# Kernel tuning notes

Hardware: AMD Instinct MI355X
Metric: run time of the kernel (lower is better)

## Reference

```python
import jax, jax.numpy as jnp
import numpy as np

NEG_SLOPE = 0.2
BN_EPS = 1e-5
NUM_GRAPHS = 500


def gat_conv(x, src, dst, W, att_src, att_dst, bias, num_nodes):
    # x: [N, Fin], W: [Fin, H*C], att_*: [H, C], bias: [H*C]
    H, C = att_src.shape
    xh = (x @ W).reshape(num_nodes, H, C)                      # [N,H,C]
    a_src = jnp.einsum('nhc,hc->nh', xh, att_src)              # [N,H]
    a_dst = jnp.einsum('nhc,hc->nh', xh, att_dst)              # [N,H]
    e = jax.nn.leaky_relu(a_src[src] + a_dst[dst], NEG_SLOPE)  # [E,H]
    m = jax.ops.segment_max(e, dst, num_segments=num_nodes)    # [N,H]
    m = jnp.where(jnp.isfinite(m), m, 0.0)
    ee = jnp.exp(e - m[dst])
    s = jax.ops.segment_sum(ee, dst, num_segments=num_nodes)   # [N,H]
    alpha = ee / (s[dst] + 1e-16)                              # [E,H]
    out = jax.ops.segment_sum(alpha[:, :, None] * xh[src], dst,
                              num_segments=num_nodes)          # [N,H,C]
    return out.reshape(num_nodes, H * C) + bias


def bn_eval(x, gamma, beta, rmean, rvar):
    return (x - rmean) * jax.lax.rsqrt(rvar + BN_EPS) * gamma + beta


def setup_inputs() -> dict:
    key = jax.random.key(0)
    ks = jax.random.split(key, 24)
    N, E, F_in, A = 50000, 1600000, 32, 16
    inp = {
        'x': jax.random.normal(ks[0], (N, F_in), jnp.float32),
        'edge_index': jax.random.randint(ks[1], (2, E), 0, N, jnp.int32),
        'batch': jnp.sort(jax.random.randint(ks[2], (N,), 0, NUM_GRAPHS, jnp.int32)),
        'W1': jax.random.normal(ks[3], (F_in, 64), jnp.float32) * 0.1,
        'att_src1': jax.random.normal(ks[4], (4, 16), jnp.float32) * 0.1,
        'att_dst1': jax.random.normal(ks[5], (4, 16), jnp.float32) * 0.1,
        'b1': jnp.zeros((64,), jnp.float32),
        'bn1_g': jnp.ones((64,), jnp.float32),
        'bn1_b': jnp.zeros((64,), jnp.float32),
        'bn1_rm': jax.random.normal(ks[6], (64,), jnp.float32) * 0.1,
        'bn1_rv': jax.random.uniform(ks[7], (64,), jnp.float32) + 0.5,
        'W2': jax.random.normal(ks[8], (64, 128), jnp.float32) * 0.1,
        'att_src2': jax.random.normal(ks[9], (4, 32), jnp.float32) * 0.1,
        'att_dst2': jax.random.normal(ks[10], (4, 32), jnp.float32) * 0.1,
        'b2': jnp.zeros((128,), jnp.float32),
        'bn2_g': jnp.ones((128,), jnp.float32),
        'bn2_b': jnp.zeros((128,), jnp.float32),
        'bn2_rm': jax.random.normal(ks[11], (128,), jnp.float32) * 0.1,
        'bn2_rv': jax.random.uniform(ks[12], (128,), jnp.float32) + 0.5,
        # attention pooling gate
        'gate_W': jax.random.normal(ks[13], (128, 1), jnp.float32) * 0.1,
        'gate_b': jnp.zeros((1,), jnp.float32),
        # heads
        'fc1_W': jax.random.normal(ks[14], (128, 32), jnp.float32) * 0.1,
        'fc1_b': jnp.zeros((32,), jnp.float32),
        'val_W': jax.random.normal(ks[15], (32, 1), jnp.float32) * 0.1,
        'val_b': jnp.zeros((1,), jnp.float32),
        'adv_W': jax.random.normal(ks[16], (32, A), jnp.float32) * 0.1,
        'adv_b': jnp.zeros((A,), jnp.float32),
    }
    return inp


def reference(x, edge_index, batch, W1, att_src1, att_dst1, b1,
              bn1_g, bn1_b, bn1_rm, bn1_rv,
              W2, att_src2, att_dst2, b2,
              bn2_g, bn2_b, bn2_rm, bn2_rv,
              gate_W, gate_b, fc1_W, fc1_b,
              val_W, val_b, adv_W, adv_b):
    N = x.shape[0]
    # GATConv default add_self_loops=True
    loop = jnp.arange(N, dtype=edge_index.dtype)
    src = jnp.concatenate([edge_index[0], loop])
    dst = jnp.concatenate([edge_index[1], loop])

    h = gat_conv(x, src, dst, W1, att_src1, att_dst1, b1, N)
    h = jax.nn.relu(bn_eval(h, bn1_g, bn1_b, bn1_rm, bn1_rv))
    h = gat_conv(h, src, dst, W2, att_src2, att_dst2, b2, N)
    h = jax.nn.relu(bn_eval(h, bn2_g, bn2_b, bn2_rm, bn2_rv))

    # AttentionalAggregation: softmax(gate) over nodes per graph, weighted sum
    gate = h @ gate_W + gate_b                                  # [N,1]
    gmax = jax.ops.segment_max(gate, batch, num_segments=NUM_GRAPHS)
    gmax = jnp.where(jnp.isfinite(gmax), gmax, 0.0)
    ge = jnp.exp(gate - gmax[batch])
    gs = jax.ops.segment_sum(ge, batch, num_segments=NUM_GRAPHS)
    w = ge / (gs[batch] + 1e-16)                                # [N,1]
    pooled = jax.ops.segment_sum(w * h, batch, num_segments=NUM_GRAPHS)  # [G,128]

    z = jax.nn.relu(pooled @ fc1_W + fc1_b)
    value = z @ val_W + val_b                                   # [G,1]
    adv = z @ adv_W + adv_b                                     # [G,A]
    return value + (adv - adv.mean(axis=1, keepdims=True))
```

## Files before the change

### kernel.cpp

```cpp
#include <hip/hip_runtime.h>
#include <hip/hip_fp16.h>
#include <math.h>

#define NEG_SLOPE 0.2f
#define BN_EPS_F 1e-5f
#define NUM_G 500
#define NBUK_MAX 128
#define CHUNK 4096

typedef float v2f __attribute__((ext_vector_type(2)));

__device__ __forceinline__ float leaky(float x){ return x > 0.f ? x : NEG_SLOPE*x; }
__device__ __forceinline__ float bcast(float v, int k){
  return __int_as_float(__builtin_amdgcn_readlane(__float_as_int(v), k));
}

#define HB 256
#define BB 64
#define L1B 512
__global__ __launch_bounds__(256) void fused_hist_lin1_kernel(
    const int* __restrict__ edst, int E, int* __restrict__ bukcnt,
    int bshift, int nbuk,
    const int* __restrict__ batch, int* __restrict__ gcnt,
    const float* __restrict__ x, const float* __restrict__ W,
    const float* __restrict__ att_s, const float* __restrict__ att_d,
    unsigned char* __restrict__ xh, float* __restrict__ a_src, float* __restrict__ a_dst, int N)
{
  __shared__ int lhist[NUM_G];
  int t = threadIdx.x;
  int bid = blockIdx.x;
  if (bid < HB) {
    if (t < NBUK_MAX) lhist[t] = 0;
    __syncthreads();
    int i = bid*256 + t, stride = HB*256;
    for (; i < E; i += stride) atomicAdd(&lhist[edst[i] >> bshift], 1);
    __syncthreads();
    if (t < nbuk && lhist[t]) atomicAdd(&bukcnt[t], lhist[t]);
  } else if (bid < HB + BB) {
    for (int i = t; i < NUM_G; i += 256) lhist[i] = 0;
    __syncthreads();
    int i = (bid-HB)*256 + t, stride = BB*256;
    for (; i < N; i += stride) atomicAdd(&lhist[batch[i]], 1);
    __syncthreads();
    for (int i = t; i < NUM_G; i += 256) if (lhist[i]) atomicAdd(&gcnt[i], lhist[i]);
  } else {
    int lane = t & 63;
    int wid  = ((bid - HB - BB)*256 + t) >> 6;
    int nw   = (L1B*256) >> 6;
    float w[32];
    #pragma unroll
    for (int k = 0; k < 32; ++k) w[k] = W[k*64 + lane];
    float asv = att_s[lane], adv = att_d[lane];
    for (int n = wid; n < N; n += nw) {
      float xv = (lane < 32) ? x[(size_t)n*32 + lane] : 0.f;
      float acc = 0.f;
      #pragma unroll
      for (int k = 0; k < 32; ++k) acc = fmaf(bcast(xv, k), w[k], acc);
      float sv = acc*asv, dv = acc*adv;
      #pragma unroll
      for (int m = 1; m < 16; m <<= 1) { sv += __shfl_xor(sv, m); dv += __shfl_xor(dv, m); }
      float accp = __shfl_xor(acc, 1);
      if ((lane & 1) == 0) {
        int p = __builtin_amdgcn_cvt_pk_fp8_f32(acc, accp, 0, false);
        *(unsigned short*)(xh + (size_t)n*64 + lane) = (unsigned short)(p & 0xffff);
      }
      if ((lane & 15) == 0) { a_src[n*4 + (lane>>4)] = sv; a_dst[n*4 + (lane>>4)] = dv; }
    }
  }
}

__global__ __launch_bounds__(1024) void exscan2_kernel(
    const int* __restrict__ in0, int* __restrict__ out0, int n0,
    const int* __restrict__ in1, int* __restrict__ out1, int n1)
{
  const int* in  = blockIdx.x ? in1  : in0;
  int*       out = blockIdx.x ? out1 : out0;
  int        n   = blockIdx.x ? n1   : n0;
  __shared__ int part[1024];
  int t = threadIdx.x;
  int per = (n + 1023) >> 10;
  int lo = t*per, hi = lo + per; if (lo > n) lo = n; if (hi > n) hi = n;
  int s = 0;
  for (int i = lo; i < hi; ++i) s += in[i];
  part[t] = s;
  __syncthreads();
  for (int ofs = 1; ofs < 1024; ofs <<= 1) {
    int v = (t >= ofs) ? part[t-ofs] : 0;
    __syncthreads();
    part[t] += v;
    __syncthreads();
  }
  int base = part[t] - s;
  for (int i = lo; i < hi; ++i) { out[i] = base; base += in[i]; }
  if (t == 1023) out[n] = part[1023];
}

__global__ __launch_bounds__(256) void binscat_kernel(
    const int* __restrict__ esrc, const int* __restrict__ edst, int E,
    const int* __restrict__ bukoff, int* __restrict__ bukcur,
    int2* __restrict__ pairs, int bshift, int nbuk)
{
  __shared__ int hist[NBUK_MAX];
  __shared__ int loffs[NBUK_MAX];
  __shared__ int gbase[NBUK_MAX];
  __shared__ int2 stage[CHUNK];
  int t = threadIdx.x;
  for (int c0 = blockIdx.x*CHUNK; c0 < E; c0 += gridDim.x*CHUNK) {
    int cnt = E - c0; if (cnt > CHUNK) cnt = CHUNK;
    if (t < NBUK_MAX) hist[t] = 0;
    __syncthreads();
    for (int i = t; i < cnt; i += 256)
      atomicAdd(&hist[edst[c0+i] >> bshift], 1);
    __syncthreads();
    int cb = (t < nbuk) ? hist[t] : 0;
    for (int ofs = 1; ofs < nbuk; ofs <<= 1) {
      int v = (t < nbuk && t >= ofs) ? hist[t-ofs] : 0;
      __syncthreads();
      if (t < nbuk) hist[t] += v;
      __syncthreads();
    }
    if (t < nbuk) {
      int lo = hist[t] - cb;
      loffs[t] = lo;
      int base = atomicAdd(&bukcur[t], cb);
      gbase[t] = bukoff[t] + base - lo;
    }
    __syncthreads();
    if (t < nbuk) hist[t] = 0;
    __syncthreads();
    for (int i = t; i < cnt; i += 256) {
      int s = esrc[c0+i], d = edst[c0+i];
      int b = d >> bshift;
      int r = atomicAdd(&hist[b], 1);
      stage[loffs[b] + r] = make_int2(s, d);
    }
    __syncthreads();
    for (int j = t; j < cnt; j += 256) {
      int2 p = stage[j];
      pairs[gbase[p.y >> bshift] + j] = p;
    }
    __syncthreads();
  }
}

__global__ __launch_bounds__(512) void bucket_csr_kernel(
    const int2* __restrict__ pairs, const int* __restrict__ bukoff,
    int* __restrict__ off, int* __restrict__ csr, int N, int E, int bshift)
{
  __shared__ int cnt[1024];
  __shared__ int cur[1024];
  __shared__ int part[512];
  int b = blockIdx.x, t = threadIdx.x;
  int base = b << bshift;
  int bnodes = 1 << bshift;
  int nlocal = N - base; if (nlocal > bnodes) nlocal = bnodes;
  int lo = bukoff[b], hi = bukoff[b+1];
  int gb = lo;
  for (int i = t; i < bnodes; i += 512) cnt[i] = 0;
  __syncthreads();
  for (int i = lo + t; i < hi; i += 512) atomicAdd(&cnt[pairs[i].y - base], 1);
  __syncthreads();
  int Wc = bnodes >> 9;
  int mys = 0;
  for (int j = 0; j < Wc; ++j) mys += cnt[t*Wc + j];
  part[t] = mys;
  __syncthreads();
  for (int ofs = 1; ofs < 512; ofs <<= 1) {
    int v = (t >= ofs) ? part[t-ofs] : 0;
    __syncthreads();
    part[t] += v;
    __syncthreads();
  }
  int ex = part[t] - mys;
  for (int j = 0; j < Wc; ++j) { int c = cnt[t*Wc + j]; cnt[t*Wc + j] = ex; ex += c; }
  __syncthreads();
  for (int i = t; i < nlocal; i += 512) off[base + i] = gb + cnt[i];
  if (b == 0 && t == 0) off[N] = E;
  for (int i = t; i < bnodes; i += 512) cur[i] = 0;
  __syncthreads();
  for (int i = lo + t; i < hi; i += 512) {
    int2 p = pairs[i];
    int l = p.y - base;
    int pos = gb + cnt[l] + atomicAdd(&cur[l], 1);
    csr[pos] = p.x;
  }
}

__global__ __launch_bounds__(256) void gat_agg1_kernel(
    const unsigned char* __restrict__ xh, const float* __restrict__ a_src, const float* __restrict__ a_dst,
    const int* __restrict__ off, const int* __restrict__ csr,
    const float* __restrict__ bias, const float* __restrict__ bng, const float* __restrict__ bnb,
    const float* __restrict__ bnrm, const float* __restrict__ bnrv,
    float* __restrict__ hout, int N)
{
  int lane = threadIdx.x & 63;
  int wid  = (blockIdx.x * blockDim.x + threadIdx.x) >> 6;
  int nw   = (gridDim.x * blockDim.x) >> 6;
  int g  = lane >> 4;
  int li = lane & 15;
  int c0 = li * 4;
  int h  = li >> 2;
  float sc[4], of[4];
  #pragma unroll
  for (int j = 0; j < 4; ++j) {
    sc[j] = rsqrtf(bnrv[c0+j]+BN_EPS_F) * bng[c0+j];
    of[j] = bias[c0+j]*sc[j] + bnb[c0+j] - bnrm[c0+j]*sc[j];
  }
  for (int n = wid; n < N; n += nw) {
    int lo = off[n], hi = off[n+1];
    float adh = a_dst[n*4+h];
    float es  = __expf(leaky(a_src[n*4+h] + adh));
    float acc0=0.f, acc1=0.f, acc2=0.f, acc3=0.f, ssum=0.f;
    for (int e = lo; e < hi; e += 4) {
      int ee = e + g; bool ok = ee < hi;
      int s = __builtin_nontemporal_load(csr + (ok ? ee : lo));
      float a = a_src[s*4+h];
      unsigned int rw = *(const unsigned int*)(xh + (size_t)s*64 + c0);
      float w = ok ? __expf(leaky(a+adh)) : 0.f;
      ssum += w;
      v2f flo = __builtin_amdgcn_cvt_pk_f32_fp8(rw, false);
      v2f fhi = __builtin_amdgcn_cvt_pk_f32_fp8(rw, true);
      acc0 = fmaf(w, flo.x, acc0); acc1 = fmaf(w, flo.y, acc1);
      acc2 = fmaf(w, fhi.x, acc2); acc3 = fmaf(w, fhi.y, acc3);
    }
    #pragma unroll
    for (int m = 16; m < 64; m <<= 1) {
      acc0 += __shfl_xor(acc0, m); acc1 += __shfl_xor(acc1, m);
      acc2 += __shfl_xor(acc2, m); acc3 += __shfl_xor(acc3, m);
      ssum += __shfl_xor(ssum, m);
    }
    unsigned int rw = *(const unsigned int*)(xh + (size_t)n*64 + c0);
    v2f flo = __builtin_amdgcn_cvt_pk_f32_fp8(rw, false);
    v2f fhi = __builtin_amdgcn_cvt_pk_f32_fp8(rw, true);
    acc0 = fmaf(es, flo.x, acc0); acc1 = fmaf(es, flo.y, acc1);
    acc2 = fmaf(es, fhi.x, acc2); acc3 = fmaf(es, fhi.y, acc3);
    ssum += es;
    float inv = 1.f / (ssum + 1e-16f);
    if (g == 0) {
      float4 r;
      r.x = fmaxf(fmaf(acc0*inv, sc[0], of[0]), 0.f);
      r.y = fmaxf(fmaf(acc1*inv, sc[1], of[1]), 0.f);
      r.z = fmaxf(fmaf(acc2*inv, sc[2], of[2]), 0.f);
      r.w = fmaxf(fmaf(acc3*inv, sc[3], of[3]), 0.f);
      *(float4*)(hout + (size_t)n*64 + c0) = r;
    }
  }
}

__global__ __launch_bounds__(256) void lin2_kernel(
    const float* __restrict__ hin, const float* __restrict__ W,
    const float* __restrict__ att_s, const float* __restrict__ att_d,
    unsigned char* __restrict__ xh, float* __restrict__ a_src, float* __restrict__ a_dst, int N)
{
  int lane = threadIdx.x & 63;
  int wid  = (blockIdx.x * blockDim.x + threadIdx.x) >> 6;
  int nw   = (gridDim.x * blockDim.x) >> 6;
  float wa[64], wb[64];
  #pragma unroll
  for (int k = 0; k < 64; ++k) { wa[k] = W[k*128 + lane]; wb[k] = W[k*128 + 64 + lane]; }
  float asa = att_s[lane], ada = att_d[lane];
  float asb = att_s[64+lane], adb = att_d[64+lane];
  for (int n = wid; n < N; n += nw) {
    float hv = hin[(size_t)n*64 + lane];
    float a0 = 0.f, a1 = 0.f;
    #pragma unroll
    for (int k = 0; k < 64; ++k) {
      float h = bcast(hv, k);
      a0 = fmaf(h, wa[k], a0); a1 = fmaf(h, wb[k], a1);
    }
    float sva = a0*asa, dva = a0*ada, svb = a1*asb, dvb = a1*adb;
    #pragma unroll
    for (int m = 1; m < 32; m <<= 1) {
      sva += __shfl_xor(sva, m); dva += __shfl_xor(dva, m);
      svb += __shfl_xor(svb, m); dvb += __shfl_xor(dvb, m);
    }
    float b0 = __shfl_xor(a0, 1);
    float b1 = __shfl_xor(a1, 1);
    if ((lane & 1) == 0) {
      int p0 = __builtin_amdgcn_cvt_pk_fp8_f32(a0, b0, 0, false);
      int p1 = __builtin_amdgcn_cvt_pk_fp8_f32(a1, b1, 0, false);
      *(unsigned short*)(xh + (size_t)n*128 + lane)      = (unsigned short)(p0 & 0xffff);
      *(unsigned short*)(xh + (size_t)n*128 + 64 + lane) = (unsigned short)(p1 & 0xffff);
    }
    if ((lane & 31) == 0) {
      int hh = lane >> 5;
      a_src[n*4 + hh] = sva;     a_dst[n*4 + hh] = dva;
      a_src[n*4 + 2 + hh] = svb; a_dst[n*4 + 2 + hh] = dvb;
    }
  }
}

__global__ __launch_bounds__(256) void gat_agg2_kernel(
    const unsigned char* __restrict__ xh, const float* __restrict__ a_src, const float* __restrict__ a_dst,
    const int* __restrict__ off, const int* __restrict__ csr,
    const float* __restrict__ bias, const float* __restrict__ bng, const float* __restrict__ bnb,
    const float* __restrict__ bnrm, const float* __restrict__ bnrv,
    const float* __restrict__ gateW, const float* __restrict__ gateB,
    float* __restrict__ hout, float* __restrict__ gate, int N)
{
  int lane = threadIdx.x & 63;
  int wid  = (blockIdx.x * blockDim.x + threadIdx.x) >> 6;
  int nw   = (gridDim.x * blockDim.x) >> 6;
  int g  = lane >> 4;
  int li = lane & 15;
  int c0 = li * 8;
  int h  = li >> 2;
  float sc[8], of[8], gw[8];
  #pragma unroll
  for (int j = 0; j < 8; ++j) {
    sc[j] = rsqrtf(bnrv[c0+j]+BN_EPS_F) * bng[c0+j];
    of[j] = bias[c0+j]*sc[j] + bnb[c0+j] - bnrm[c0+j]*sc[j];
    gw[j] = gateW[c0+j];
  }
  float gb = gateB[0];
  for (int n = wid; n < N; n += nw) {
    int lo = off[n], hi = off[n+1];
    float adh = a_dst[n*4+h];
    float es  = __expf(leaky(a_src[n*4+h] + adh));
    float acc0=0.f, acc1=0.f, acc2=0.f, acc3=0.f;
    float acc4=0.f, acc5=0.f, acc6=0.f, acc7=0.f, ssum=0.f;
    for (int e = lo; e < hi; e += 4) {
      int ee = e + g; bool ok = ee < hi;
      int s = __builtin_nontemporal_load(csr + (ok ? ee : lo));
      float a = a_src[s*4+h];
      int2 rv = *(const int2*)(xh + (size_t)s*128 + c0);
      float w = ok ? __expf(leaky(a+adh)) : 0.f;
      ssum += w;
      v2f f0 = __builtin_amdgcn_cvt_pk_f32_fp8((unsigned)rv.x, false);
      v2f f1 = __builtin_amdgcn_cvt_pk_f32_fp8((unsigned)rv.x, true);
      v2f f2 = __builtin_amdgcn_cvt_pk_f32_fp8((unsigned)rv.y, false);
      v2f f3 = __builtin_amdgcn_cvt_pk_f32_fp8((unsigned)rv.y, true);
      acc0 = fmaf(w, f0.x, acc0); acc1 = fmaf(w, f0.y, acc1);
      acc2 = fmaf(w, f1.x, acc2); acc3 = fmaf(w, f1.y, acc3);
      acc4 = fmaf(w, f2.x, acc4); acc5 = fmaf(w, f2.y, acc5);
      acc6 = fmaf(w, f3.x, acc6); acc7 = fmaf(w, f3.y, acc7);
    }
    #pragma unroll
    for (int m = 16; m < 64; m <<= 1) {
      acc0 += __shfl_xor(acc0, m); acc1 += __shfl_xor(acc1, m);
      acc2 += __shfl_xor(acc2, m); acc3 += __shfl_xor(acc3, m);
      acc4 += __shfl_xor(acc4, m); acc5 += __shfl_xor(acc5, m);
      acc6 += __shfl_xor(acc6, m); acc7 += __shfl_xor(acc7, m);
      ssum += __shfl_xor(ssum, m);
    }
    int2 rv = *(const int2*)(xh + (size_t)n*128 + c0);
    v2f f0 = __builtin_amdgcn_cvt_pk_f32_fp8((unsigned)rv.x, false);
    v2f f1 = __builtin_amdgcn_cvt_pk_f32_fp8((unsigned)rv.x, true);
    v2f f2 = __builtin_amdgcn_cvt_pk_f32_fp8((unsigned)rv.y, false);
    v2f f3 = __builtin_amdgcn_cvt_pk_f32_fp8((unsigned)rv.y, true);
    acc0 = fmaf(es, f0.x, acc0); acc1 = fmaf(es, f0.y, acc1);
    acc2 = fmaf(es, f1.x, acc2); acc3 = fmaf(es, f1.y, acc3);
    acc4 = fmaf(es, f2.x, acc4); acc5 = fmaf(es, f2.y, acc5);
    acc6 = fmaf(es, f3.x, acc6); acc7 = fmaf(es, f3.y, acc7);
    ssum += es;
    float inv = 1.f / (ssum + 1e-16f);
    float r0 = fmaxf(fmaf(acc0*inv, sc[0], of[0]), 0.f);
    float r1 = fmaxf(fmaf(acc1*inv, sc[1], of[1]), 0.f);
    float r2 = fmaxf(fmaf(acc2*inv, sc[2], of[2]), 0.f);
    float r3 = fmaxf(fmaf(acc3*inv, sc[3], of[3]), 0.f);
    float r4 = fmaxf(fmaf(acc4*inv, sc[4], of[4]), 0.f);
    float r5 = fmaxf(fmaf(acc5*inv, sc[5], of[5]), 0.f);
    float r6 = fmaxf(fmaf(acc6*inv, sc[6], of[6]), 0.f);
    float r7 = fmaxf(fmaf(acc7*inv, sc[7], of[7]), 0.f);
    if (g == 0) {
      float4 w0 = make_float4(r0, r1, r2, r3);
      float4 w1 = make_float4(r4, r5, r6, r7);
      *(float4*)(hout + (size_t)n*128 + c0)     = w0;
      *(float4*)(hout + (size_t)n*128 + c0 + 4) = w1;
    }
    float gl = r0*gw[0] + r1*gw[1] + r2*gw[2] + r3*gw[3]
             + r4*gw[4] + r5*gw[5] + r6*gw[6] + r7*gw[7];
    #pragma unroll
    for (int m = 1; m < 16; m <<= 1) gl += __shfl_xor(gl, m);
    if (lane == 0) gate[n] = gl + gb;
  }
}

__global__ __launch_bounds__(128) void pool_kernel(
    const float* __restrict__ h2, const float* __restrict__ gate, const int* __restrict__ goff,
    const float* __restrict__ fc1W, const float* __restrict__ fc1b,
    const float* __restrict__ valW, const float* __restrict__ valb,
    const float* __restrict__ advW, const float* __restrict__ advb,
    float* __restrict__ out)
{
  int g = blockIdx.x, t = threadIdx.x;
  int lo = goff[g], hi = goff[g+1];
  __shared__ float red[2];
  __shared__ float pld[128];
  __shared__ float zs[32];
  __shared__ float sval;
  __shared__ float adv_s[16];

  float m = -3.4e38f;
  for (int n = lo+t; n < hi; n += 128) m = fmaxf(m, gate[n]);
  #pragma unroll
  for (int msk = 1; msk < 64; msk <<= 1) m = fmaxf(m, __shfl_xor(m, msk));
  if ((t & 63) == 0) red[t >> 6] = m;
  __syncthreads();
  m = fmaxf(red[0], red[1]);
  __syncthreads();
  float sl = 0.f;
  for (int n = lo+t; n < hi; n += 128) sl += __expf(gate[n]-m);
  #pragma unroll
  for (int msk = 1; msk < 64; msk <<= 1) sl += __shfl_xor(sl, msk);
  if ((t & 63) == 0) red[t >> 6] = sl;
  __syncthreads();
  float s = red[0] + red[1];
  float acc = 0.f;
  for (int n = lo; n < hi; ++n) {
    float w = __expf(gate[n]-m);
    acc += w * h2[(size_t)n*128 + t];
  }
  pld[t] = acc / (s + 1e-16f);
  __syncthreads();
  if (t < 32) {
    float z = fc1b[t];
    #pragma unroll 4
    for (int k = 0; k < 128; ++k) z += pld[k]*fc1W[k*32 + t];
    zs[t] = fmaxf(z, 0.f);
  }
  __syncthreads();
  if (t < 32) {
    float pv = zs[t]*valW[t];
    #pragma unroll
    for (int msk = 1; msk < 32; msk <<= 1) pv += __shfl_xor(pv, msk);
    if (t == 0) sval = pv + valb[0];
  }
  if (t < 16) {
    float a = advb[t];
    #pragma unroll
    for (int k = 0; k < 32; ++k) a += zs[k]*advW[k*16 + t];
    adv_s[t] = a;
  }
  __syncthreads();
  if (t < 16) {
    float amean = adv_s[t];
    #pragma unroll
    for (int msk = 1; msk < 16; msk <<= 1) amean += __shfl_xor(amean, msk);
    amean *= (1.f/16.f);
    out[g*16 + t] = sval + adv_s[t] - amean;
  }
}

extern "C" void kernel_launch(void* const* d_in, const int* in_sizes, int n_in,
                              void* d_out, int out_size, void* d_ws, size_t ws_size,
                              hipStream_t stream)
{
  const float* x     = (const float*)d_in[0];
  const int*   eidx  = (const int*)  d_in[1];
  const int*   batch = (const int*)  d_in[2];
  const float* W1    = (const float*)d_in[3];
  const float* as1w  = (const float*)d_in[4];
  const float* ad1w  = (const float*)d_in[5];
  const float* b1    = (const float*)d_in[6];
  const float* bn1g  = (const float*)d_in[7];
  const float* bn1b  = (const float*)d_in[8];
  const float* bn1rm = (const float*)d_in[9];
  const float* bn1rv = (const float*)d_in[10];
  const float* W2    = (const float*)d_in[11];
  const float* as2w  = (const float*)d_in[12];
  const float* ad2w  = (const float*)d_in[13];
  const float* b2    = (const float*)d_in[14];
  const float* bn2g  = (const float*)d_in[15];
  const float* bn2b  = (const float*)d_in[16];
  const float* bn2rm = (const float*)d_in[17];
  const float* bn2rv = (const float*)d_in[18];
  const float* gateW = (const float*)d_in[19];
  const float* gateB = (const float*)d_in[20];
  const float* fc1W  = (const float*)d_in[21];
  const float* fc1b  = (const float*)d_in[22];
  const float* valW  = (const float*)d_in[23];
  const float* valb  = (const float*)d_in[24];
  const float* advW  = (const float*)d_in[25];
  const float* advb  = (const float*)d_in[26];

  int N = in_sizes[0] / 32;
  int E = in_sizes[1] / 2;
  const int* esrc = eidx;
  const int* edst = eidx + E;

  int bshift = 9;
  while ((((N - 1) >> bshift) + 1) > NBUK_MAX) ++bshift;
  int nbuk = ((N - 1) >> bshift) + 1;

  float* ws = (float*)d_ws;
  size_t o = 0;
  unsigned char* xh1q = (unsigned char*)(ws + o); o += (size_t)N*16;
  unsigned char* xh2q = (unsigned char*)(ws + o); o += (size_t)N*32;
  float* as1 = ws + o; o += (size_t)N*4;
  float* ad1 = ws + o; o += (size_t)N*4;
  float* as2 = ws + o; o += (size_t)N*4;
  float* ad2 = ws + o; o += (size_t)N*4;
  float* h1  = ws + o; o += (size_t)N*64;
  float* h2  = ws + o; o += (size_t)N*128;
  float* gate = ws + o; o += (size_t)N;
  if (o & 1) ++o;
  int2* pairs = (int2*)(ws + o); o += (size_t)E*2;
  int* ib     = (int*)(ws + o);
  int* gcnt   = ib;
  int* bukcnt = ib + 512;
  int* bukcur = ib + 640;
  size_t zcnt = 768;
  int* off    = ib + zcnt;
  int* goff   = off + (N+1);
  int* bukoff = goff + (NUM_G+1);
  int* csr    = bukoff + (NBUK_MAX+1);

  hipMemsetAsync(gcnt, 0, zcnt*sizeof(int), stream);

  fused_hist_lin1_kernel<<<HB+BB+L1B, 256, 0, stream>>>(
      edst, E, bukcnt, bshift, nbuk, batch, gcnt,
      x, W1, as1w, ad1w, xh1q, as1, ad1, N);
  exscan2_kernel<<<2, 1024, 0, stream>>>(bukcnt, bukoff, nbuk, gcnt, goff, NUM_G);
  int nchunk = (E + CHUNK - 1) / CHUNK;
  binscat_kernel<<<nchunk, 256, 0, stream>>>(esrc, edst, E, bukoff, bukcur, pairs, bshift, nbuk);
  bucket_csr_kernel<<<nbuk, 512, 0, stream>>>(pairs, bukoff, off, csr, N, E, bshift);
  gat_agg1_kernel<<<2048, 256, 0, stream>>>(xh1q, as1, ad1, off, csr,
      b1, bn1g, bn1b, bn1rm, bn1rv, h1, N);
  lin2_kernel<<<1024, 256, 0, stream>>>(h1, W2, as2w, ad2w, xh2q, as2, ad2, N);
  gat_agg2_kernel<<<2048, 256, 0, stream>>>(xh2q, as2, ad2, off, csr,
      b2, bn2g, bn2b, bn2rm, bn2rv, gateW, gateB, h2, gate, N);
  pool_kernel<<<NUM_G, 128, 0, stream>>>(h2, gate, goff, fc1W, fc1b, valW, valb, advW, advb,
      (float*)d_out);
}
```

Before: 281.6 us.

## Precompute per-edge attention weights in fp16 before aggregation kernels

Adds an edge_wgt_kernel that computes exp(leaky(a_src[s]+a_dst[n])) per edge and head once, stores it as fp16 in CSR order, and has both aggregation kernels read it instead of gathering a_src and computing exp per lane. The aggregation loop gets sequential fp16 loads in place of a random gather of a_src. Layer-1 aggregation is also reshaped to 8 edges per iteration with 8 channels per lane. This adds two extra kernel launches, each re-gathering a_src, plus a write and read of a 12.8MB weight array. It also rounds the weights to fp16 precision.

Measured after the change: 292.6 us. 1.04x slower.

```diff
diff --git a/kernel.cpp b/kernel.cpp
--- a/kernel.cpp
+++ b/kernel.cpp
@@ -186,9 +186,30 @@
   }
 }
 
+__global__ __launch_bounds__(256) void edge_wgt_kernel(
+    const int* __restrict__ csr, const int* __restrict__ off,
+    const float* __restrict__ a_src, const float* __restrict__ a_dst,
+    __half* __restrict__ wgt, int N)
+{
+  int lane = threadIdx.x & 63;
+  int wid  = (blockIdx.x * blockDim.x + threadIdx.x) >> 6;
+  int nw   = (gridDim.x * blockDim.x) >> 6;
+  int h  = lane & 3;
+  int eo = lane >> 2;
+  for (int n = wid; n < N; n += nw) {
+    int lo = off[n], hi = off[n+1];
+    float adh = a_dst[n*4 + h];
+    for (int e = lo + eo; e < hi; e += 16) {
+      int s = csr[e];
+      float w = __expf(leaky(a_src[s*4 + h] + adh));
+      wgt[(size_t)e*4 + h] = __float2half(w);
+    }
+  }
+}
+
 __global__ __launch_bounds__(256) void gat_agg1_kernel(
     const unsigned char* __restrict__ xh, const float* __restrict__ a_src, const float* __restrict__ a_dst,
-    const int* __restrict__ off, const int* __restrict__ csr,
+    const int* __restrict__ off, const int* __restrict__ csr, const __half* __restrict__ wgt,
     const float* __restrict__ bias, const float* __restrict__ bng, const float* __restrict__ bnb,
     const float* __restrict__ bnrm, const float* __restrict__ bnrv,
     float* __restrict__ hout, int N)
@@ -196,13 +217,13 @@
   int lane = threadIdx.x & 63;
   int wid  = (blockIdx.x * blockDim.x + threadIdx.x) >> 6;
   int nw   = (gridDim.x * blockDim.x) >> 6;
-  int g  = lane >> 4;
-  int li = lane & 15;
-  int c0 = li * 4;
-  int h  = li >> 2;
-  float sc[4], of[4];
+  int g  = lane >> 3;
+  int li = lane & 7;
+  int c0 = li * 8;
+  int h  = li >> 1;
+  float sc[8], of[8];
   #pragma unroll
-  for (int j = 0; j < 4; ++j) {
+  for (int j = 0; j < 8; ++j) {
     sc[j] = rsqrtf(bnrv[c0+j]+BN_EPS_F) * bng[c0+j];
     of[j] = bias[c0+j]*sc[j] + bnb[c0+j] - bnrm[c0+j]*sc[j];
   }
@@ -210,39 +231,56 @@
     int lo = off[n], hi = off[n+1];
     float adh = a_dst[n*4+h];
     float es  = __expf(leaky(a_src[n*4+h] + adh));
-    float acc0=0.f, acc1=0.f, acc2=0.f, acc3=0.f, ssum=0.f;
-    for (int e = lo; e < hi; e += 4) {
+    float acc0=0.f, acc1=0.f, acc2=0.f, acc3=0.f;
+    float acc4=0.f, acc5=0.f, acc6=0.f, acc7=0.f, ssum=0.f;
+    for (int e = lo; e < hi; e += 8) {
       int ee = e + g; bool ok = ee < hi;
-      int s = __builtin_nontemporal_load(csr + (ok ? ee : lo));
-      float a = a_src[s*4+h];
-      unsigned int rw = *(const unsigned int*)(xh + (size_t)s*64 + c0);
-      float w = ok ? __expf(leaky(a+adh)) : 0.f;
+      int idx = ok ? ee : lo;
+      int s = __builtin_nontemporal_load(csr + idx);
+      float wv = __half2float(wgt[(size_t)idx*4 + h]);
+      float w = ok ? wv : 0.f;
+      int2 rv = *(const int2*)(xh + (size_t)s*64 + c0);
       ssum += w;
-      v2f flo = __builtin_amdgcn_cvt_pk_f32_fp8(rw, false);
-      v2f fhi = __builtin_amdgcn_cvt_pk_f32_fp8(rw, true);
-      acc0 = fmaf(w, flo.x, acc0); acc1 = fmaf(w, flo.y, acc1);
-      acc2 = fmaf(w, fhi.x, acc2); acc3 = fmaf(w, fhi.y, acc3);
-    }
-    #pragma unroll
-    for (int m = 16; m < 64; m <<= 1) {
+      v2f f0 = __builtin_amdgcn_cvt_pk_f32_fp8((unsigned)rv.x, false);
+      v2f f1 = __builtin_amdgcn_cvt_pk_f32_fp8((unsigned)rv.x, true);
+      v2f f2 = __builtin_amdgcn_cvt_pk_f32_fp8((unsigned)rv.y, false);
+      v2f f3 = __builtin_amdgcn_cvt_pk_f32_fp8((unsigned)rv.y, true);
+      acc0 = fmaf(w, f0.x, acc0); acc1 = fmaf(w, f0.y, acc1);
+      acc2 = fmaf(w, f1.x, acc2); acc3 = fmaf(w, f1.y, acc3);
+      acc4 = fmaf(w, f2.x, acc4); acc5 = fmaf(w, f2.y, acc5);
+      acc6 = fmaf(w, f3.x, acc6); acc7 = fmaf(w, f3.y, acc7);
+    }
+    #pragma unroll
+    for (int m = 8; m < 64; m <<= 1) {
       acc0 += __shfl_xor(acc0, m); acc1 += __shfl_xor(acc1, m);
       acc2 += __shfl_xor(acc2, m); acc3 += __shfl_xor(acc3, m);
+      acc4 += __shfl_xor(acc4, m); acc5 += __shfl_xor(acc5, m);
+      acc6 += __shfl_xor(acc6, m); acc7 += __shfl_xor(acc7, m);
       ssum += __shfl_xor(ssum, m);
     }
-    unsigned int rw = *(const unsigned int*)(xh + (size_t)n*64 + c0);
-    v2f flo = __builtin_amdgcn_cvt_pk_f32_fp8(rw, false);
-    v2f fhi = __builtin_amdgcn_cvt_pk_f32_fp8(rw, true);
-    acc0 = fmaf(es, flo.x, acc0); acc1 = fmaf(es, flo.y, acc1);
-    acc2 = fmaf(es, fhi.x, acc2); acc3 = fmaf(es, fhi.y, acc3);
+    int2 rv = *(const int2*)(xh + (size_t)n*64 + c0);
+    v2f f0 = __builtin_amdgcn_cvt_pk_f32_fp8((unsigned)rv.x, false);
+    v2f f1 = __builtin_amdgcn_cvt_pk_f32_fp8((unsigned)rv.x, true);
+    v2f f2 = __builtin_amdgcn_cvt_pk_f32_fp8((unsigned)rv.y, false);
+    v2f f3 = __builtin_amdgcn_cvt_pk_f32_fp8((unsigned)rv.y, true);
+    acc0 = fmaf(es, f0.x, acc0); acc1 = fmaf(es, f0.y, acc1);
+    acc2 = fmaf(es, f1.x, acc2); acc3 = fmaf(es, f1.y, acc3);
+    acc4 = fmaf(es, f2.x, acc4); acc5 = fmaf(es, f2.y, acc5);
+    acc6 = fmaf(es, f3.x, acc6); acc7 = fmaf(es, f3.y, acc7);
     ssum += es;
     float inv = 1.f / (ssum + 1e-16f);
     if (g == 0) {
-      float4 r;
-      r.x = fmaxf(fmaf(acc0*inv, sc[0], of[0]), 0.f);
-      r.y = fmaxf(fmaf(acc1*inv, sc[1], of[1]), 0.f);
-      r.z = fmaxf(fmaf(acc2*inv, sc[2], of[2]), 0.f);
-      r.w = fmaxf(fmaf(acc3*inv, sc[3], of[3]), 0.f);
-      *(float4*)(hout + (size_t)n*64 + c0) = r;
+      float4 w0, w1;
+      w0.x = fmaxf(fmaf(acc0*inv, sc[0], of[0]), 0.f);
+      w0.y = fmaxf(fmaf(acc1*inv, sc[1], of[1]), 0.f);
+      w0.z = fmaxf(fmaf(acc2*inv, sc[2], of[2]), 0.f);
+      w0.w = fmaxf(fmaf(acc3*inv, sc[3], of[3]), 0.f);
+      w1.x = fmaxf(fmaf(acc4*inv, sc[4], of[4]), 0.f);
+      w1.y = fmaxf(fmaf(acc5*inv, sc[5], of[5]), 0.f);
+      w1.z = fmaxf(fmaf(acc6*inv, sc[6], of[6]), 0.f);
+      w1.w = fmaxf(fmaf(acc7*inv, sc[7], of[7]), 0.f);
+      *(float4*)(hout + (size_t)n*64 + c0)     = w0;
+      *(float4*)(hout + (size_t)n*64 + c0 + 4) = w1;
     }
   }
 }
@@ -292,7 +330,7 @@
 
 __global__ __launch_bounds__(256) void gat_agg2_kernel(
     const unsigned char* __restrict__ xh, const float* __restrict__ a_src, const float* __restrict__ a_dst,
-    const int* __restrict__ off, const int* __restrict__ csr,
+    const int* __restrict__ off, const int* __restrict__ csr, const __half* __restrict__ wgt,
     const float* __restrict__ bias, const float* __restrict__ bng, const float* __restrict__ bnb,
     const float* __restrict__ bnrm, const float* __restrict__ bnrv,
     const float* __restrict__ gateW, const float* __restrict__ gateB,
@@ -321,10 +359,11 @@
     float acc4=0.f, acc5=0.f, acc6=0.f, acc7=0.f, ssum=0.f;
     for (int e = lo; e < hi; e += 4) {
       int ee = e + g; bool ok = ee < hi;
-      int s = __builtin_nontemporal_load(csr + (ok ? ee : lo));
-      float a = a_src[s*4+h];
+      int idx = ok ? ee : lo;
+      int s = __builtin_nontemporal_load(csr + idx);
+      float wv = __half2float(wgt[(size_t)idx*4 + h]);
+      float w = ok ? wv : 0.f;
       int2 rv = *(const int2*)(xh + (size_t)s*128 + c0);
-      float w = ok ? __expf(leaky(a+adh)) : 0.f;
       ssum += w;
       v2f f0 = __builtin_amdgcn_cvt_pk_f32_fp8((unsigned)rv.x, false);
       v2f f1 = __builtin_amdgcn_cvt_pk_f32_fp8((unsigned)rv.x, true);
@@ -496,6 +535,7 @@
   float* gate = ws + o; o += (size_t)N;
   if (o & 1) ++o;
   int2* pairs = (int2*)(ws + o); o += (size_t)E*2;
+  __half* wgt = (__half*)(ws + o); o += (size_t)E*2;
   int* ib     = (int*)(ws + o);
   int* gcnt   = ib;
   int* bukcnt = ib + 512;
@@ -515,10 +555,12 @@
   int nchunk = (E + CHUNK - 1) / CHUNK;
   binscat_kernel<<<nchunk, 256, 0, stream>>>(esrc, edst, E, bukoff, bukcur, pairs, bshift, nbuk);
   bucket_csr_kernel<<<nbuk, 512, 0, stream>>>(pairs, bukoff, off, csr, N, E, bshift);
-  gat_agg1_kernel<<<2048, 256, 0, stream>>>(xh1q, as1, ad1, off, csr,
+  edge_wgt_kernel<<<2048, 256, 0, stream>>>(csr, off, as1, ad1, wgt, N);
+  gat_agg1_kernel<<<2048, 256, 0, stream>>>(xh1q, as1, ad1, off, csr, wgt,
       b1, bn1g, bn1b, bn1rm, bn1rv, h1, N);
   lin2_kernel<<<1024, 256, 0, stream>>>(h1, W2, as2w, ad2w, xh2q, as2, ad2, N);
-  gat_agg2_kernel<<<2048, 256, 0, stream>>>(xh2q, as2, ad2, off, csr,
+  edge_wgt_kernel<<<2048, 256, 0, stream>>>(csr, off, as2, ad2, wgt, N);
+  gat_agg2_kernel<<<2048, 256, 0, stream>>>(xh2q, as2, ad2, off, csr, wgt,
       b2, bn2g, bn2b, bn2rm, bn2rv, gateW, gateB, h2, gate, N);
   pool_kernel<<<NUM_G, 128, 0, stream>>>(h2, gate, goff, fc1W, fc1b, valW, valb, advW, advb,
       (float*)d_out);
```

## Aggregate raw features before the linear projection in both GAT layers

Applied to the files above, without the earlier changes.

Uses the linearity of the projection to reorder each GAT layer: the layer input (x for layer 1, h1 for layer 2) is gathered in fp8 with per-head softmax weights, and the weight matrix is applied afterwards per node from shared memory. This halves the bytes gathered per edge in both aggregations and removes the fp8 projected-feature writes from lin2, which now only computes attention scores. In exchange each lane keeps four per-head accumulator sets (four times the exp and FMA work per edge) and does a per-node matmul from LDS. The 32KB W2 tile in shared memory may also reduce occupancy in the second aggregation.

Measured after the change: 362.2 us. 28.6% more time.

```diff
diff --git a/kernel.cpp b/kernel.cpp
--- a/kernel.cpp
+++ b/kernel.cpp
@@ -24,7 +24,7 @@
     const int* __restrict__ batch, int* __restrict__ gcnt,
     const float* __restrict__ x, const float* __restrict__ W,
     const float* __restrict__ att_s, const float* __restrict__ att_d,
-    unsigned char* __restrict__ xh, float* __restrict__ a_src, float* __restrict__ a_dst, int N)
+    unsigned char* __restrict__ x8, float* __restrict__ a_src, float* __restrict__ a_dst, int N)
 {
   __shared__ int lhist[NUM_G];
   int t = threadIdx.x;
@@ -59,10 +59,10 @@
       float sv = acc*asv, dv = acc*adv;
       #pragma unroll
       for (int m = 1; m < 16; m <<= 1) { sv += __shfl_xor(sv, m); dv += __shfl_xor(dv, m); }
-      float accp = __shfl_xor(acc, 1);
-      if ((lane & 1) == 0) {
-        int p = __builtin_amdgcn_cvt_pk_fp8_f32(acc, accp, 0, false);
-        *(unsigned short*)(xh + (size_t)n*64 + lane) = (unsigned short)(p & 0xffff);
+      float xp = __shfl_xor(xv, 1);
+      if (lane < 32 && (lane & 1) == 0) {
+        int p = __builtin_amdgcn_cvt_pk_fp8_f32(xv, xp, 0, false);
+        *(unsigned short*)(x8 + (size_t)n*32 + lane) = (unsigned short)(p & 0xffff);
       }
       if ((lane & 15) == 0) { a_src[n*4 + (lane>>4)] = sv; a_dst[n*4 + (lane>>4)] = dv; }
     }
@@ -187,62 +187,90 @@
 }
 
 __global__ __launch_bounds__(256) void gat_agg1_kernel(
-    const unsigned char* __restrict__ xh, const float* __restrict__ a_src, const float* __restrict__ a_dst,
+    const unsigned char* __restrict__ x8, const float* __restrict__ a_src, const float* __restrict__ a_dst,
     const int* __restrict__ off, const int* __restrict__ csr,
+    const float* __restrict__ W1,
     const float* __restrict__ bias, const float* __restrict__ bng, const float* __restrict__ bnb,
     const float* __restrict__ bnrm, const float* __restrict__ bnrv,
-    float* __restrict__ hout, int N)
-{
-  int lane = threadIdx.x & 63;
-  int wid  = (blockIdx.x * blockDim.x + threadIdx.x) >> 6;
+    float* __restrict__ h1, unsigned char* __restrict__ h18, int N)
+{
+  __shared__ float W1s[32*64];
+  __shared__ float aggs[4][4][32];
+  int t = threadIdx.x;
+  for (int i = t; i < 32*64; i += 256) W1s[i] = W1[i];
+  __syncthreads();
+  int lane = t & 63;
+  int wv   = t >> 6;
+  int wid  = (blockIdx.x * blockDim.x + t) >> 6;
   int nw   = (gridDim.x * blockDim.x) >> 6;
-  int g  = lane >> 4;
-  int li = lane & 15;
+  int g  = lane >> 3;
+  int li = lane & 7;
   int c0 = li * 4;
-  int h  = li >> 2;
-  float sc[4], of[4];
-  #pragma unroll
-  for (int j = 0; j < 4; ++j) {
-    sc[j] = rsqrtf(bnrv[c0+j]+BN_EPS_F) * bng[c0+j];
-    of[j] = bias[c0+j]*sc[j] + bnb[c0+j] - bnrm[c0+j]*sc[j];
-  }
+  int o  = lane;
+  int oh = o >> 4;
+  float sc  = rsqrtf(bnrv[o]+BN_EPS_F) * bng[o];
+  float ofc = bias[o]*sc + bnb[o] - bnrm[o]*sc;
+  const float4* as4 = (const float4*)a_src;
+  const float4* ad4 = (const float4*)a_dst;
   for (int n = wid; n < N; n += nw) {
     int lo = off[n], hi = off[n+1];
-    float adh = a_dst[n*4+h];
-    float es  = __expf(leaky(a_src[n*4+h] + adh));
-    float acc0=0.f, acc1=0.f, acc2=0.f, acc3=0.f, ssum=0.f;
-    for (int e = lo; e < hi; e += 4) {
+    float4 adn = ad4[n];
+    float a0=0,a1=0,a2=0,a3=0, b0=0,b1=0,b2=0,b3=0, c1=0,c2=0,c3=0,cc0=0, d0=0,d1=0,d2=0,d3=0;
+    float s0=0,s1=0,s2=0,s3=0;
+    for (int e = lo; e < hi; e += 8) {
       int ee = e + g; bool ok = ee < hi;
-      int s = __builtin_nontemporal_load(csr + (ok ? ee : lo));
-      float a = a_src[s*4+h];
-      unsigned int rw = *(const unsigned int*)(xh + (size_t)s*64 + c0);
-      float w = ok ? __expf(leaky(a+adh)) : 0.f;
-      ssum += w;
+      int idx = ok ? ee : lo;
+      int s = __builtin_nontemporal_load(csr + idx);
+      float4 av = as4[s];
+      unsigned int rw = *(const unsigned int*)(x8 + (size_t)s*32 + c0);
+      float w0 = ok ? __expf(leaky(av.x+adn.x)) : 0.f;
+      float w1 = ok ? __expf(leaky(av.y+adn.y)) : 0.f;
+      float w2 = ok ? __expf(leaky(av.z+adn.z)) : 0.f;
+      float w3 = ok ? __expf(leaky(av.w+adn.w)) : 0.f;
+      s0+=w0; s1+=w1; s2+=w2; s3+=w3;
       v2f flo = __builtin_amdgcn_cvt_pk_f32_fp8(rw, false);
       v2f fhi = __builtin_amdgcn_cvt_pk_f32_fp8(rw, true);
-      acc0 = fmaf(w, flo.x, acc0); acc1 = fmaf(w, flo.y, acc1);
-      acc2 = fmaf(w, fhi.x, acc2); acc3 = fmaf(w, fhi.y, acc3);
-    }
-    #pragma unroll
-    for (int m = 16; m < 64; m <<= 1) {
-      acc0 += __shfl_xor(acc0, m); acc1 += __shfl_xor(acc1, m);
-      acc2 += __shfl_xor(acc2, m); acc3 += __shfl_xor(acc3, m);
-      ssum += __shfl_xor(ssum, m);
-    }
-    unsigned int rw = *(const unsigned int*)(xh + (size_t)n*64 + c0);
+      a0=fmaf(w0,flo.x,a0); a1=fmaf(w0,flo.y,a1); a2=fmaf(w0,fhi.x,a2); a3=fmaf(w0,fhi.y,a3);
+      b0=fmaf(w1,flo.x,b0); b1=fmaf(w1,flo.y,b1); b2=fmaf(w1,fhi.x,b2); b3=fmaf(w1,fhi.y,b3);
+      cc0=fmaf(w2,flo.x,cc0); c1=fmaf(w2,flo.y,c1); c2=fmaf(w2,fhi.x,c2); c3=fmaf(w2,fhi.y,c3);
+      d0=fmaf(w3,flo.x,d0); d1=fmaf(w3,flo.y,d1); d2=fmaf(w3,fhi.x,d2); d3=fmaf(w3,fhi.y,d3);
+    }
+    #pragma unroll
+    for (int m = 8; m < 64; m <<= 1) {
+      a0+=__shfl_xor(a0,m); a1+=__shfl_xor(a1,m); a2+=__shfl_xor(a2,m); a3+=__shfl_xor(a3,m);
+      b0+=__shfl_xor(b0,m); b1+=__shfl_xor(b1,m); b2+=__shfl_xor(b2,m); b3+=__shfl_xor(b3,m);
+      cc0+=__shfl_xor(cc0,m); c1+=__shfl_xor(c1,m); c2+=__shfl_xor(c2,m); c3+=__shfl_xor(c3,m);
+      d0+=__shfl_xor(d0,m); d1+=__shfl_xor(d1,m); d2+=__shfl_xor(d2,m); d3+=__shfl_xor(d3,m);
+      s0+=__shfl_xor(s0,m); s1+=__shfl_xor(s1,m); s2+=__shfl_xor(s2,m); s3+=__shfl_xor(s3,m);
+    }
+    float4 asn = as4[n];
+    float e0=__expf(leaky(asn.x+adn.x)), e1=__expf(leaky(asn.y+adn.y));
+    float e2=__expf(leaky(asn.z+adn.z)), e3=__expf(leaky(asn.w+adn.w));
+    unsigned int rw = *(const unsigned int*)(x8 + (size_t)n*32 + c0);
     v2f flo = __builtin_amdgcn_cvt_pk_f32_fp8(rw, false);
     v2f fhi = __builtin_amdgcn_cvt_pk_f32_fp8(rw, true);
-    acc0 = fmaf(es, flo.x, acc0); acc1 = fmaf(es, flo.y, acc1);
-    acc2 = fmaf(es, fhi.x, acc2); acc3 = fmaf(es, fhi.y, acc3);
-    ssum += es;
-    float inv = 1.f / (ssum + 1e-16f);
+    a0=fmaf(e0,flo.x,a0); a1=fmaf(e0,flo.y,a1); a2=fmaf(e0,fhi.x,a2); a3=fmaf(e0,fhi.y,a3);
+    b0=fmaf(e1,flo.x,b0); b1=fmaf(e1,flo.y,b1); b2=fmaf(e1,fhi.x,b2); b3=fmaf(e1,fhi.y,b3);
+    cc0=fmaf(e2,flo.x,cc0); c1=fmaf(e2,flo.y,c1); c2=fmaf(e2,fhi.x,c2); c3=fmaf(e2,fhi.y,c3);
+    d0=fmaf(e3,flo.x,d0); d1=fmaf(e3,flo.y,d1); d2=fmaf(e3,fhi.x,d2); d3=fmaf(e3,fhi.y,d3);
+    s0+=e0; s1+=e1; s2+=e2; s3+=e3;
+    float i0=1.f/(s0+1e-16f), i1=1.f/(s1+1e-16f), i2=1.f/(s2+1e-16f), i3=1.f/(s3+1e-16f);
     if (g == 0) {
-      float4 r;
-      r.x = fmaxf(fmaf(acc0*inv, sc[0], of[0]), 0.f);
-      r.y = fmaxf(fmaf(acc1*inv, sc[1], of[1]), 0.f);
-      r.z = fmaxf(fmaf(acc2*inv, sc[2], of[2]), 0.f);
-      r.w = fmaxf(fmaf(acc3*inv, sc[3], of[3]), 0.f);
-      *(float4*)(hout + (size_t)n*64 + c0) = r;
+      aggs[wv][0][c0]=a0*i0; aggs[wv][0][c0+1]=a1*i0; aggs[wv][0][c0+2]=a2*i0; aggs[wv][0][c0+3]=a3*i0;
+      aggs[wv][1][c0]=b0*i1; aggs[wv][1][c0+1]=b1*i1; aggs[wv][1][c0+2]=b2*i1; aggs[wv][1][c0+3]=b3*i1;
+      aggs[wv][2][c0]=cc0*i2; aggs[wv][2][c0+1]=c1*i2; aggs[wv][2][c0+2]=c2*i2; aggs[wv][2][c0+3]=c3*i2;
+      aggs[wv][3][c0]=d0*i3; aggs[wv][3][c0+1]=d1*i3; aggs[wv][3][c0+2]=d2*i3; aggs[wv][3][c0+3]=d3*i3;
+    }
+    float val = 0.f;
+    #pragma unroll 8
+    for (int c = 0; c < 32; ++c)
+      val = fmaf(aggs[wv][oh][c], W1s[c*64 + o], val);
+    float r = fmaxf(fmaf(val, sc, ofc), 0.f);
+    h1[(size_t)n*64 + o] = r;
+    float rp = __shfl_xor(r, 1);
+    if ((lane & 1) == 0) {
+      int p = __builtin_amdgcn_cvt_pk_fp8_f32(r, rp, 0, false);
+      *(unsigned short*)(h18 + (size_t)n*64 + o) = (unsigned short)(p & 0xffff);
     }
   }
 }
@@ -250,7 +278,7 @@
 __global__ __launch_bounds__(256) void lin2_kernel(
     const float* __restrict__ hin, const float* __restrict__ W,
     const float* __restrict__ att_s, const float* __restrict__ att_d,
-    unsigned char* __restrict__ xh, float* __restrict__ a_src, float* __restrict__ a_dst, int N)
+    float* __restrict__ a_src, float* __restrict__ a_dst, int N)
 {
   int lane = threadIdx.x & 63;
   int wid  = (blockIdx.x * blockDim.x + threadIdx.x) >> 6;
@@ -274,14 +302,6 @@
       sva += __shfl_xor(sva, m); dva += __shfl_xor(dva, m);
       svb += __shfl_xor(svb, m); dvb += __shfl_xor(dvb, m);
     }
-    float b0 = __shfl_xor(a0, 1);
-    float b1 = __shfl_xor(a1, 1);
-    if ((lane & 1) == 0) {
-      int p0 = __builtin_amdgcn_cvt_pk_fp8_f32(a0, b0, 0, false);
-      int p1 = __builtin_amdgcn_cvt_pk_fp8_f32(a1, b1, 0, false);
-      *(unsigned short*)(xh + (size_t)n*128 + lane)      = (unsigned short)(p0 & 0xffff);
-      *(unsigned short*)(xh + (size_t)n*128 + 64 + lane) = (unsigned short)(p1 & 0xffff);
-    }
     if ((lane & 31) == 0) {
       int hh = lane >> 5;
       a_src[n*4 + hh] = sva;     a_dst[n*4 + hh] = dva;
@@ -291,87 +311,97 @@
 }
 
 __global__ __launch_bounds__(256) void gat_agg2_kernel(
-    const unsigned char* __restrict__ xh, const float* __restrict__ a_src, const float* __restrict__ a_dst,
+    const unsigned char* __restrict__ h18, const float* __restrict__ a_src, const float* __restrict__ a_dst,
     const int* __restrict__ off, const int* __restrict__ csr,
+    const float* __restrict__ W2,
     const float* __restrict__ bias, const float* __restrict__ bng, const float* __restrict__ bnb,
     const float* __restrict__ bnrm, const float* __restrict__ bnrv,
     const float* __restrict__ gateW, const float* __restrict__ gateB,
     float* __restrict__ hout, float* __restrict__ gate, int N)
 {
-  int lane = threadIdx.x & 63;
-  int wid  = (blockIdx.x * blockDim.x + threadIdx.x) >> 6;
+  __shared__ float W2s[64*128];
+  __shared__ float aggs[4][4][64];
+  int t = threadIdx.x;
+  for (int i = t; i < 64*128; i += 256) W2s[i] = W2[i];
+  __syncthreads();
+  int lane = t & 63;
+  int wv   = t >> 6;
+  int wid  = (blockIdx.x * blockDim.x + t) >> 6;
   int nw   = (gridDim.x * blockDim.x) >> 6;
   int g  = lane >> 4;
   int li = lane & 15;
-  int c0 = li * 8;
-  int h  = li >> 2;
-  float sc[8], of[8], gw[8];
-  #pragma unroll
-  for (int j = 0; j < 8; ++j) {
-    sc[j] = rsqrtf(bnrv[c0+j]+BN_EPS_F) * bng[c0+j];
-    of[j] = bias[c0+j]*sc[j] + bnb[c0+j] - bnrm[c0+j]*sc[j];
-    gw[j] = gateW[c0+j];
-  }
-  float gb = gateB[0];
+  int c0 = li * 4;
+  int o1 = lane, o2 = lane + 64;
+  int h1o = o1 >> 5, h2o = o2 >> 5;
+  float sc1  = rsqrtf(bnrv[o1]+BN_EPS_F) * bng[o1];
+  float of1  = bias[o1]*sc1 + bnb[o1] - bnrm[o1]*sc1;
+  float sc2  = rsqrtf(bnrv[o2]+BN_EPS_F) * bng[o2];
+  float of2  = bias[o2]*sc2 + bnb[o2] - bnrm[o2]*sc2;
+  float gw1 = gateW[o1], gw2 = gateW[o2], gb = gateB[0];
+  const float4* as4 = (const float4*)a_src;
+  const float4* ad4 = (const float4*)a_dst;
   for (int n = wid; n < N; n += nw) {
     int lo = off[n], hi = off[n+1];
-    float adh = a_dst[n*4+h];
-    float es  = __expf(leaky(a_src[n*4+h] + adh));
-    float acc0=0.f, acc1=0.f, acc2=0.f, acc3=0.f;
-    float acc4=0.f, acc5=0.f, acc6=0.f, acc7=0.f, ssum=0.f;
+    float4 adn = ad4[n];
+    float a0=0,a1=0,a2=0,a3=0, b0=0,b1=0,b2=0,b3=0, cc0=0,c1=0,c2=0,c3=0, d0=0,d1=0,d2=0,d3=0;
+    float s0=0,s1=0,s2=0,s3=0;
     for (int e = lo; e < hi; e += 4) {
       int ee = e + g; bool ok = ee < hi;
-      int s = __builtin_nontemporal_load(csr + (ok ? ee : lo));
-      float a = a_src[s*4+h];
-      int2 rv = *(const int2*)(xh + (size_t)s*128 + c0);
-      float w = ok ? __expf(leaky(a+adh)) : 0.f;
-      ssum += w;
-      v2f f0 = __builtin_amdgcn_cvt_pk_f32_fp8((unsigned)rv.x, false);
-      v2f f1 = __builtin_amdgcn_cvt_pk_f32_fp8((unsigned)rv.x, true);
-      v2f f2 = __builtin_amdgcn_cvt_pk_f32_fp8((unsigned)rv.y, false);
-      v2f f3 = __builtin_amdgcn_cvt_pk_f32_fp8((unsigned)rv.y, true);
-      acc0 = fmaf(w, f0.x, acc0); acc1 = fmaf(w, f0.y, acc1);
-      acc2 = fmaf(w, f1.x, acc2); acc3 = fmaf(w, f1.y, acc3);
-      acc4 = fmaf(w, f2.x, acc4); acc5 = fmaf(w, f2.y, acc5);
-      acc6 = fmaf(w, f3.x, acc6); acc7 = fmaf(w, f3.y, acc7);
+      int idx = ok ? ee : lo;
+      int s = __builtin_nontemporal_load(csr + idx);
+      float4 av = as4[s];
+      unsigned int rw = *(const unsigned int*)(h18 + (size_t)s*64 + c0);
+      float w0 = ok ? __expf(leaky(av.x+adn.x)) : 0.f;
+      float w1 = ok ? __expf(leaky(av.y+adn.y)) : 0.f;
+      float w2 = ok ? __expf(leaky(av.z+adn.z)) : 0.f;
+      float w3 = ok ? __expf(leaky(av.w+adn.w)) : 0.f;
+      s0+=w0; s1+=w1; s2+=w2; s3+=w3;
+      v2f flo = __builtin_amdgcn_cvt_pk_f32_fp8(rw, false);
+      v2f fhi = __builtin_amdgcn_cvt_pk_f32_fp8(rw, true);
+      a0=fmaf(w0,flo.x,a0); a1=fmaf(w0,flo.y,a1); a2=fmaf(w0,fhi.x,a2); a3=fmaf(w0,fhi.y,a3);
+      b0=fmaf(w1,flo.x,b0); b1=fmaf(w1,flo.y,b1); b2=fmaf(w1,fhi.x,b2); b3=fmaf(w1,fhi.y,b3);
+      cc0=fmaf(w2,flo.x,cc0); c1=fmaf(w2,flo.y,c1); c2=fmaf(w2,fhi.x,c2); c3=fmaf(w2,fhi.y,c3);
+      d0=fmaf(w3,flo.x,d0); d1=fmaf(w3,flo.y,d1); d2=fmaf(w3,fhi.x,d2); d3=fmaf(w3,fhi.y,d3);
     }
     #pragma unroll
     for (int m = 16; m < 64; m <<= 1) {
-      acc0 += __shfl_xor(acc0, m); acc1 += __shfl_xor(acc1, m);
-      acc2 += __shfl_xor(acc2, m); acc3 += __shfl_xor(acc3, m);
-      acc4 += __shfl_xor(acc4, m); acc5 += __shfl_xor(acc5, m);
-      acc6 += __shfl_xor(acc6, m); acc7 += __shfl_xor(acc7, m);
-      ssum += __shfl_xor(ssum, m);
-    }
-    int2 rv = *(const int2*)(xh + (size_t)n*128 + c0);
-    v2f f0 = __builtin_amdgcn_cvt_pk_f32_fp8((unsigned)rv.x, false);
-    v2f f1 = __builtin_amdgcn_cvt_pk_f32_fp8((unsigned)rv.x, true);
-    v2f f2 = __builtin_amdgcn_cvt_pk_f32_fp8((unsigned)rv.y, false);
-    v2f f3 = __builtin_amdgcn_cvt_pk_f32_fp8((unsigned)rv.y, true);
-    acc0 = fmaf(es, f0.x, acc0); acc1 = fmaf(es, f0.y, acc1);
-    acc2 = fmaf(es, f1.x, acc2); acc3 = fmaf(es, f1.y, acc3);
-    acc4 = fmaf(es, f2.x, acc4); acc5 = fmaf(es, f2.y, acc5);
-    acc6 = fmaf(es, f3.x, acc6); acc7 = fmaf(es, f3.y, acc7);
-    ssum += es;
-    float inv = 1.f / (ssum + 1e-16f);
-    float r0 = fmaxf(fmaf(acc0*inv, sc[0], of[0]), 0.f);
-    float r1 = fmaxf(fmaf(acc1*inv, sc[1], of[1]), 0.f);
-    float r2 = fmaxf(fmaf(acc2*inv, sc[2], of[2]), 0.f);
-    float r3 = fmaxf(fmaf(acc3*inv, sc[3], of[3]), 0.f);
-    float r4 = fmaxf(fmaf(acc4*inv, sc[4], of[4]), 0.f);
-    float r5 = fmaxf(fmaf(acc5*inv, sc[5], of[5]), 0.f);
-    float r6 = fmaxf(fmaf(acc6*inv, sc[6], of[6]), 0.f);
-    float r7 = fmaxf(fmaf(acc7*inv, sc[7], of[7]), 0.f);
+      a0+=__shfl_xor(a0,m); a1+=__shfl_xor(a1,m); a2+=__shfl_xor(a2,m); a3+=__shfl_xor(a3,m);
+      b0+=__shfl_xor(b0,m); b1+=__shfl_xor(b1,m); b2+=__shfl_xor(b2,m); b3+=__shfl_xor(b3,m);
+      cc0+=__shfl_xor(cc0,m); c1+=__shfl_xor(c1,m); c2+=__shfl_xor(c2,m); c3+=__shfl_xor(c3,m);
+      d0+=__shfl_xor(d0,m); d1+=__shfl_xor(d1,m); d2+=__shfl_xor(d2,m); d3+=__shfl_xor(d3,m);
+      s0+=__shfl_xor(s0,m); s1+=__shfl_xor(s1,m); s2+=__shfl_xor(s2,m); s3+=__shfl_xor(s3,m);
+    }
+    float4 asn = as4[n];
+    float e0=__expf(leaky(asn.x+adn.x)), e1=__expf(leaky(asn.y+adn.y));
+    float e2=__expf(leaky(asn.z+adn.z)), e3=__expf(leaky(asn.w+adn.w));
+    unsigned int rw = *(const unsigned int*)(h18 + (size_t)n*64 + c0);
+    v2f flo = __builtin_amdgcn_cvt_pk_f32_fp8(rw, false);
+    v2f fhi = __builtin_amdgcn_cvt_pk_f32_fp8(rw, true);
+    a0=fmaf(e0,flo.x,a0); a1=fmaf(e0,flo.y,a1); a2=fmaf(e0,fhi.x,a2); a3=fmaf(e0,fhi.y,a3);
+    b0=fmaf(e1,flo.x,b0); b1=fmaf(e1,flo.y,b1); b2=fmaf(e1,fhi.x,b2); b3=fmaf(e1,fhi.y,b3);
+    cc0=fmaf(e2,flo.x,cc0); c1=fmaf(e2,flo.y,c1); c2=fmaf(e2,fhi.x,c2); c3=fmaf(e2,fhi.y,c3);
+    d0=fmaf(e3,flo.x,d0); d1=fmaf(e3,flo.y,d1); d2=fmaf(e3,fhi.x,d2); d3=fmaf(e3,fhi.y,d3);
+    s0+=e0; s1+=e1; s2+=e2; s3+=e3;
+    float i0=1.f/(s0+1e-16f), i1=1.f/(s1+1e-16f), i2=1.f/(s2+1e-16f), i3=1.f/(s3+1e-16f);
     if (g == 0) {
-      float4 w0 = make_float4(r0, r1, r2, r3);
-      float4 w1 = make_float4(r4, r5, r6, r7);
-      *(float4*)(hout + (size_t)n*128 + c0)     = w0;
-      *(float4*)(hout + (size_t)n*128 + c0 + 4) = w1;
-    }
-    float gl = r0*gw[0] + r1*gw[1] + r2*gw[2] + r3*gw[3]
-             + r4*gw[4] + r5*gw[5] + r6*gw[6] + r7*gw[7];
-    #pragma unroll
-    for (int m = 1; m < 16; m <<= 1) gl += __shfl_xor(gl, m);
+      aggs[wv][0][c0]=a0*i0; aggs[wv][0][c0+1]=a1*i0; aggs[wv][0][c0+2]=a2*i0; aggs[wv][0][c0+3]=a3*i0;
+      aggs[wv][1][c0]=b0*i1; aggs[wv][1][c0+1]=b1*i1; aggs[wv][1][c0+2]=b2*i1; aggs[wv][1][c0+3]=b3*i1;
+      aggs[wv][2][c0]=cc0*i2; aggs[wv][2][c0+1]=c1*i2; aggs[wv][2][c0+2]=c2*i2; aggs[wv][2][c0+3]=c3*i2;
+      aggs[wv][3][c0]=d0*i3; aggs[wv][3][c0+1]=d1*i3; aggs[wv][3][c0+2]=d2*i3; aggs[wv][3][c0+3]=d3*i3;
+    }
+    float v1 = 0.f, v2 = 0.f;
+    #pragma unroll 8
+    for (int c = 0; c < 64; ++c) {
+      v1 = fmaf(aggs[wv][h1o][c], W2s[c*128 + o1], v1);
+      v2 = fmaf(aggs[wv][h2o][c], W2s[c*128 + o2], v2);
+    }
+    float r1 = fmaxf(fmaf(v1, sc1, of1), 0.f);
+    float r2 = fmaxf(fmaf(v2, sc2, of2), 0.f);
+    hout[(size_t)n*128 + o1] = r1;
+    hout[(size_t)n*128 + o2] = r2;
+    float gl = r1*gw1 + r2*gw2;
+    #pragma unroll
+    for (int m = 1; m < 64; m <<= 1) gl += __shfl_xor(gl, m);
     if (lane == 0) gate[n] = gl + gb;
   }
 }
@@ -485,8 +515,8 @@
 
   float* ws = (float*)d_ws;
   size_t o = 0;
-  unsigned char* xh1q = (unsigned char*)(ws + o); o += (size_t)N*16;
-  unsigned char* xh2q = (unsigned char*)(ws + o); o += (size_t)N*32;
+  unsigned char* x8  = (unsigned char*)(ws + o); o += (size_t)N*8;
+  unsigned char* h18 = (unsigned char*)(ws + o); o += (size_t)N*16;
   float* as1 = ws + o; o += (size_t)N*4;
   float* ad1 = ws + o; o += (size_t)N*4;
   float* as2 = ws + o; o += (size_t)N*4;
@@ -510,15 +540,15 @@
 
   fused_hist_lin1_kernel<<<HB+BB+L1B, 256, 0, stream>>>(
       edst, E, bukcnt, bshift, nbuk, batch, gcnt,
-      x, W1, as1w, ad1w, xh1q, as1, ad1, N);
+      x, W1, as1w, ad1w, x8, as1, ad1, N);
   exscan2_kernel<<<2, 1024, 0, stream>>>(bukcnt, bukoff, nbuk, gcnt, goff, NUM_G);
   int nchunk = (E + CHUNK - 1) / CHUNK;
   binscat_kernel<<<nchunk, 256, 0, stream>>>(esrc, edst, E, bukoff, bukcur, pairs, bshift, nbuk);
   bucket_csr_kernel<<<nbuk, 512, 0, stream>>>(pairs, bukoff, off, csr, N, E, bshift);
-  gat_agg1_kernel<<<2048, 256, 0, stream>>>(xh1q, as1, ad1, off, csr,
-      b1, bn1g, bn1b, bn1rm, bn1rv, h1, N);
-  lin2_kernel<<<1024, 256, 0, stream>>>(h1, W2, as2w, ad2w, xh2q, as2, ad2, N);
-  gat_agg2_kernel<<<2048, 256, 0, stream>>>(xh2q, as2, ad2, off, csr,
+  gat_agg1_kernel<<<2048, 256, 0, stream>>>(x8, as1, ad1, off, csr, W1,
+      b1, bn1g, bn1b, bn1rm, bn1rv, h1, h18, N);
+  lin2_kernel<<<1024, 256, 0, stream>>>(h1, W2, as2w, ad2w, as2, ad2, N);
+  gat_agg2_kernel<<<2048, 256, 0, stream>>>(h18, as2, ad2, off, csr, W2,
       b2, bn2g, bn2b, bn2rm, bn2rv, gateW, gateB, h2, gate, N);
   pool_kernel<<<NUM_G, 128, 0, stream>>>(h2, gate, goff, fc1W, fc1b, valW, valb, advW, advb,
       (float*)d_out);
```
